# Kernel optimization log

Measured on AMD Instinct MI355X. Metric: run time of the kernel, lower is better.

Reference implementation:

```python
import jax, jax.numpy as jnp
import numpy as np

D_MODEL = 1024
N_HEADS = 16
D_HEAD = D_MODEL // N_HEADS


def setup_inputs() -> dict:
    key = jax.random.key(0)
    k1, k2, k3 = jax.random.split(key, 3)
    B, N = 2, 2048
    x = jax.random.normal(k1, (B, N, D_MODEL), dtype=jnp.float32)
    # torch nn.Linear(d, 3d, bias=False): y = x @ W.T ; we store W_qkv as [D, 3D]
    scale_in = 1.0 / np.sqrt(D_MODEL)
    W_qkv = jax.random.uniform(k2, (D_MODEL, 3 * D_MODEL), dtype=jnp.float32,
                               minval=-scale_in, maxval=scale_in)
    W_out = jax.random.uniform(k3, (D_MODEL, D_MODEL), dtype=jnp.float32,
                               minval=-scale_in, maxval=scale_in)
    return {"x": x, "W_qkv": W_qkv, "W_out": W_out}


def reference(x, W_qkv, W_out):
    B, N, D = x.shape
    qkv = x @ W_qkv                                    # [B, N, 3D]
    q, k, v = jnp.split(qkv, 3, axis=-1)
    # [B, N, D] -> [B, H, N, d_head]
    def heads(t):
        return t.reshape(B, N, N_HEADS, D_HEAD).transpose(0, 2, 1, 3)
    q, k, v = heads(q), heads(k), heads(v)
    scores = jnp.einsum('bhnd,bhmd->bhnm', q, k) / np.sqrt(D_HEAD)  # [B,H,N,N]
    causal_mask = jnp.triu(jnp.ones((N, N), dtype=bool), k=1)
    scores = jnp.where(causal_mask, -jnp.inf, scores)
    attn = jax.nn.softmax(scores, axis=-1)             # [B,H,N,N]
    out = jnp.einsum('bhnm,bhmd->bhnd', attn, v)       # [B,H,N,d_head]
    out = out.transpose(0, 2, 1, 3).reshape(B, N, D)
    out = out @ W_out.T if False else out @ W_out      # W_out stored [D,D], x @ W
    return out, attn
```

## Files before the change

### kernel.cpp

```cpp
#include <hip/hip_runtime.h>
#include <hip/hip_bf16.h>

typedef __bf16 bf16;
typedef __bf16 bf16x4 __attribute__((ext_vector_type(4)));
typedef __bf16 bf16x8 __attribute__((ext_vector_type(8)));
typedef float  f32x4  __attribute__((ext_vector_type(4)));

#define MFMA16(a, b, c) __builtin_amdgcn_mfma_f32_16x16x32_bf16((a), (b), (c), 0, 0, 0)

typedef const __attribute__((address_space(1))) void* gptr_t;
typedef __attribute__((address_space(3))) void* sptr_t;

__device__ __forceinline__ void load_lds16(const bf16* g, bf16* l) {
  __builtin_amdgcn_global_load_lds((gptr_t)g, (sptr_t)l, 16, 0, 0);
}

__global__ __launch_bounds__(256) void detect_dtype(const unsigned short* __restrict__ w,
                                                    int* __restrict__ flag) {
  __shared__ int cnt[256];
  int c = 0;
#pragma unroll
  for (int k = 0; k < 16; ++k) {
    unsigned short v = w[(threadIdx.x * 16 + k) * 2];
    int e = (v >> 7) & 0xFF;
    c += (e >= 90 && e <= 130) ? 1 : 0;
  }
  cnt[threadIdx.x] = c;
  __syncthreads();
  if (threadIdx.x == 0) {
    int t = 0;
    for (int i = 0; i < 256; ++i) t += cnt[i];
    *flag = (t > 2048) ? 1 : 0;
  }
}

__global__ __launch_bounds__(256) void convert_to_bf16(const void* __restrict__ in,
                                                       bf16* __restrict__ out,
                                                       const int* __restrict__ flag) {
  const int i0 = (blockIdx.x * 256 + threadIdx.x) * 8;
  if (*flag) {
    *(bf16x8*)(out + i0) = *(const bf16x8*)((const bf16*)in + i0);
  } else {
    const float* p = (const float*)in;
    float4 a = *(const float4*)(p + i0);
    float4 b = *(const float4*)(p + i0 + 4);
    bf16x8 v;
    v[0] = (bf16)a.x; v[1] = (bf16)a.y; v[2] = (bf16)a.z; v[3] = (bf16)a.w;
    v[4] = (bf16)b.x; v[5] = (bf16)b.y; v[6] = (bf16)b.z; v[7] = (bf16)b.w;
    *(bf16x8*)(out + i0) = v;
  }
}

__global__ __launch_bounds__(256) void transpose_any(const void* __restrict__ in,
                                                     bf16* __restrict__ out,
                                                     const int* __restrict__ flag,
                                                     int R, int C) {
  __shared__ bf16 t[64][65];
  const int c0 = blockIdx.x * 64, r0 = blockIdx.y * 64;
  const int tid = threadIdx.x;
  const int lc = tid & 63, lr4 = tid >> 6;
  if (*flag) {
    const bf16* p = (const bf16*)in;
#pragma unroll
    for (int i = 0; i < 16; ++i) {
      int r = i * 4 + lr4;
      t[r][lc] = p[(size_t)(r0 + r) * C + c0 + lc];
    }
  } else {
    const float* p = (const float*)in;
#pragma unroll
    for (int i = 0; i < 16; ++i) {
      int r = i * 4 + lr4;
      t[r][lc] = (bf16)p[(size_t)(r0 + r) * C + c0 + lc];
    }
  }
  __syncthreads();
#pragma unroll
  for (int i = 0; i < 16; ++i) {
    int r = i * 4 + lr4;
    out[(size_t)(c0 + r) * R + r0 + lc] = t[lc][r];
  }
}

__global__ __launch_bounds__(256) void transpose_v(const bf16* __restrict__ qkv,
                                                   bf16* __restrict__ vt) {
  __shared__ bf16 t[64][65];
  const int bh = blockIdx.y, b = bh >> 4, h = bh & 15;
  const int j0 = blockIdx.x * 64;
  const int tid = threadIdx.x;
  const int lc = tid & 63, lr4 = tid >> 6;
  const bf16* src = qkv + (size_t)b * 2048 * 3072 + 2048 + (size_t)h * 64;
#pragma unroll
  for (int i = 0; i < 16; ++i) {
    int j = i * 4 + lr4;
    t[j][lc] = src[(size_t)(j0 + j) * 3072 + lc];
  }
  __syncthreads();
  bf16* dst = vt + (size_t)bh * 64 * 2048;
#pragma unroll
  for (int i = 0; i < 16; ++i) {
    int d = i * 4 + lr4;
    dst[(size_t)d * 2048 + j0 + lc] = t[lc][d];
  }
}

template <typename CT>
__global__ __launch_bounds__(256) void gemm_bt(const bf16* __restrict__ A,
                                               const bf16* __restrict__ Bt,
                                               CT* __restrict__ C,
                                               int K, int ldc) {
  __shared__ bf16 a_lds[128 * 32];
  __shared__ bf16 b_lds[128 * 32];
  const int tid = threadIdx.x;
  const int w = tid >> 6, lane = tid & 63, l15 = lane & 15, quad = lane >> 4;
  const int wr = w >> 1, wc = w & 1;
  const int m0 = blockIdx.y * 128, n0 = blockIdx.x * 128;

  const f32x4 fz = {0.f, 0.f, 0.f, 0.f};
  f32x4 acc[4][4];
#pragma unroll
  for (int i = 0; i < 4; ++i)
#pragma unroll
    for (int j = 0; j < 4; ++j) acc[i][j] = fz;

  for (int k0 = 0; k0 < K; k0 += 32) {
#pragma unroll
    for (int i = 0; i < 2; ++i) {
      int c = tid + i * 256;
      int r = c >> 2, kk = c & 3;
      load_lds16(A + (size_t)(m0 + r) * K + k0 + kk * 8, &a_lds[c * 8]);
      load_lds16(Bt + (size_t)(n0 + r) * K + k0 + kk * 8, &b_lds[c * 8]);
    }
    __syncthreads();
    bf16x8 af[4], bfr[4];
#pragma unroll
    for (int mb = 0; mb < 4; ++mb)
      af[mb] = *(const bf16x8*)&a_lds[(wr * 64 + mb * 16 + l15) * 32 + quad * 8];
#pragma unroll
    for (int nb = 0; nb < 4; ++nb)
      bfr[nb] = *(const bf16x8*)&b_lds[(wc * 64 + nb * 16 + l15) * 32 + quad * 8];
#pragma unroll
    for (int mb = 0; mb < 4; ++mb)
#pragma unroll
      for (int nb = 0; nb < 4; ++nb)
        acc[mb][nb] = MFMA16(af[mb], bfr[nb], acc[mb][nb]);
    __syncthreads();
  }

#pragma unroll
  for (int mb = 0; mb < 4; ++mb)
#pragma unroll
    for (int nb = 0; nb < 4; ++nb) {
      int row = m0 + wr * 64 + mb * 16 + quad * 4;
      int col = n0 + wc * 64 + nb * 16 + l15;
#pragma unroll
      for (int r = 0; r < 4; ++r)
        C[(size_t)(row + r) * ldc + col] = (CT)acc[mb][nb][r];
    }
}

__device__ __forceinline__ void qk_tile(const char* kt_base, const bf16x8 (&qf)[2][2],
                                        int l15, int quad, f32x4 (&st)[8][2]) {
  const f32x4 fz = {0.f, 0.f, 0.f, 0.f};
  __builtin_amdgcn_s_setprio(1);
#pragma unroll
  for (int jb = 0; jb < 8; ++jb) {
    const char* kr = kt_base + (size_t)(jb * 16 + l15) * 6144 + quad * 16;
    bf16x8 kf0 = *(const bf16x8*)kr;
    bf16x8 kf1 = *(const bf16x8*)(kr + 64);
    st[jb][0] = MFMA16(kf0, qf[0][0], fz);
    st[jb][0] = MFMA16(kf1, qf[0][1], st[jb][0]);
    st[jb][1] = MFMA16(kf0, qf[1][0], fz);
    st[jb][1] = MFMA16(kf1, qf[1][1], st[jb][1]);
  }
  __builtin_amdgcn_s_setprio(0);
}

__global__ __launch_bounds__(256, 2) void fused_attn(const bf16* __restrict__ qkv,
                                                     const bf16* __restrict__ vt,
                                                     float* __restrict__ attn,
                                                     bf16* __restrict__ o_ws) {
  __shared__ bf16 p_lds[128 * 128];

  const int bh = blockIdx.y;
  const int b = bh >> 4, h = bh & 15;
  const int qt = (bh & 16) ? (15 - (int)blockIdx.x) : (int)blockIdx.x;
  const int tid = threadIdx.x;
  const int w = tid >> 6, lane = tid & 63, l15 = lane & 15, quad = lane >> 4;
  const int q0 = qt * 128;

  const char* qkvb = (const char*)qkv;
  const size_t kbyte0 = ((size_t)b * 2048 * 3072 + 1024 + (size_t)h * 64) * 2;
  const char* vtb = (const char*)vt + ((size_t)bh * 64) * 2048 * 2;

  for (int kt = qt + 1; kt < 16; ++kt) {
    float* abase = attn + ((size_t)bh << 22) + (size_t)q0 * 2048 + kt * 128;
    const f32x4 z4 = {0.f, 0.f, 0.f, 0.f};
#pragma unroll
    for (int it = 0; it < 16; ++it) {
      const int il = it * 8 + w * 2 + (lane >> 5);
      __builtin_nontemporal_store(z4, (f32x4*)(abase + (size_t)il * 2048 + (lane & 31) * 4));
    }
  }

  bf16x8 qf[2][2];
#pragma unroll
  for (int ib = 0; ib < 2; ++ib)
#pragma unroll
    for (int ks = 0; ks < 2; ++ks) {
      const bf16* qp = qkv + ((size_t)b * 2048 + q0 + w * 32 + ib * 16 + l15) * 3072
                       + h * 64 + ks * 32 + quad * 8;
      bf16x8 v = *(const bf16x8*)qp;
      bf16x8 sv;
#pragma unroll
      for (int u = 0; u < 8; ++u) sv[u] = (bf16)((float)v[u] * 0.125f);
      qf[ib][ks] = sv;
    }

  float m_run[2] = {-3e38f, -3e38f};
  float l_run[2] = {0.f, 0.f};

  for (int kt = 0; kt <= qt; ++kt) {
    f32x4 st[8][2];
    qk_tile(qkvb + kbyte0 + (size_t)kt * 128 * 6144, qf, l15, quad, st);

    const bool diag = (kt == qt);
#pragma unroll
    for (int ib = 0; ib < 2; ++ib) {
      const int ig = q0 + w * 32 + ib * 16 + l15;
      float tmax = -3e38f;
#pragma unroll
      for (int jb = 0; jb < 8; ++jb)
#pragma unroll
        for (int r = 0; r < 4; ++r) {
          const int jg = kt * 128 + jb * 16 + quad * 4 + r;
          float s = st[jb][ib][r];
          if (diag && jg > ig) { s = -3e38f; st[jb][ib][r] = s; }
          tmax = fmaxf(tmax, s);
        }
      tmax = fmaxf(tmax, __shfl_xor(tmax, 16));
      tmax = fmaxf(tmax, __shfl_xor(tmax, 32));
      const float mnew = fmaxf(m_run[ib], tmax);
      float tsum = 0.f;
#pragma unroll
      for (int jb = 0; jb < 8; ++jb)
#pragma unroll
        for (int r = 0; r < 4; ++r) {
          const float s = st[jb][ib][r];
          tsum += (s > -1e38f) ? __expf(s - mnew) : 0.f;
        }
      tsum += __shfl_xor(tsum, 16);
      tsum += __shfl_xor(tsum, 32);
      l_run[ib] = l_run[ib] * __expf(m_run[ib] - mnew) + tsum;
      m_run[ib] = mnew;
    }
  }

  const float invl[2] = {1.f / l_run[0], 1.f / l_run[1]};

  f32x4 oacc[2][4];
#pragma unroll
  for (int ib = 0; ib < 2; ++ib)
#pragma unroll
    for (int db = 0; db < 4; ++db) {
      const f32x4 fz = {0.f, 0.f, 0.f, 0.f};
      oacc[ib][db] = fz;
    }

  for (int kt = 0; kt <= qt; ++kt) {
    f32x4 st[8][2];
    qk_tile(qkvb + kbyte0 + (size_t)kt * 128 * 6144, qf, l15, quad, st);

    const bool diag = (kt == qt);
#pragma unroll
    for (int ib = 0; ib < 2; ++ib) {
      const int ig = q0 + w * 32 + ib * 16 + l15;
      const int il = w * 32 + ib * 16 + l15;
#pragma unroll
      for (int jb = 0; jb < 8; ++jb) {
        bf16x4 pk;
#pragma unroll
        for (int r = 0; r < 4; ++r) {
          const int jg = kt * 128 + jb * 16 + quad * 4 + r;
          float p = __expf(st[jb][ib][r] - m_run[ib]) * invl[ib];
          if (diag && jg > ig) p = 0.f;
          pk[r] = (bf16)p;
        }
        *(bf16x4*)((char*)p_lds + il * 256 + ((jb * 32 + quad * 8) ^ ((il & 7) << 4))) = pk;
      }
    }

    bf16x8 vfr[4][4];
#pragma unroll
    for (int js = 0; js < 4; ++js)
#pragma unroll
      for (int db = 0; db < 4; ++db) {
        const int dl = db * 16 + l15;
        vfr[js][db] = *(const bf16x8*)(vtb + (size_t)dl * 4096 + kt * 256 + js * 64 + quad * 16);
      }

    {
      float* abase = attn + ((size_t)bh << 22) + (size_t)q0 * 2048 + kt * 128;
#pragma unroll
      for (int it = 0; it < 16; ++it) {
        const int il = w * 32 + it * 2 + (lane >> 5);
        const int jb4 = (lane & 31) * 8;
        bf16x4 pv = *(const bf16x4*)((char*)p_lds + il * 256 + (jb4 ^ ((il & 7) << 4)));
        f32x4 f = {(float)pv[0], (float)pv[1], (float)pv[2], (float)pv[3]};
        __builtin_nontemporal_store(f, (f32x4*)(abase + (size_t)il * 2048 + (lane & 31) * 4));
      }
    }

    __builtin_amdgcn_s_setprio(1);
#pragma unroll
    for (int js = 0; js < 4; ++js) {
      bf16x8 pa[2];
#pragma unroll
      for (int ib = 0; ib < 2; ++ib) {
        const int il = w * 32 + ib * 16 + l15;
        pa[ib] = *(const bf16x8*)((char*)p_lds + il * 256 + ((js * 64 + quad * 16) ^ ((il & 7) << 4)));
      }
#pragma unroll
      for (int ib = 0; ib < 2; ++ib)
#pragma unroll
        for (int db = 0; db < 4; ++db)
          oacc[ib][db] = MFMA16(pa[ib], vfr[js][db], oacc[ib][db]);
    }
    __builtin_amdgcn_s_setprio(0);
  }

#pragma unroll
  for (int ib = 0; ib < 2; ++ib)
#pragma unroll
    for (int db = 0; db < 4; ++db)
#pragma unroll
      for (int r = 0; r < 4; ++r) {
        const int ig = q0 + w * 32 + ib * 16 + quad * 4 + r;
        const int dg = h * 64 + db * 16 + l15;
        o_ws[((size_t)b * 2048 + ig) * 1024 + dg] = (bf16)oacc[ib][db][r];
      }
}

extern "C" void kernel_launch(void* const* d_in, const int* in_sizes, int n_in,
                              void* d_out, int out_size, void* d_ws, size_t ws_size,
                              hipStream_t stream) {
  const void* x_raw = d_in[0];
  const void* w_qkv = d_in[1];
  const void* w_out = d_in[2];
  float* out  = (float*)d_out;
  float* attn = out + 4194304;

  bf16* ws     = (bf16*)d_ws;
  bf16* qkv_ws = ws;
  bf16* x_bf   = ws + 12582912;
  bf16* vt_ws  = ws + 12582912;
  bf16* woT    = ws + 12582912;
  bf16* wqkvT  = ws + 16777216;
  bf16* o_ws   = ws + 16777216;
  int*  flag   = (int*)(ws + 20971520);

  detect_dtype<<<1, 256, 0, stream>>>((const unsigned short*)w_qkv, flag);
  convert_to_bf16<<<2048, 256, 0, stream>>>(x_raw, x_bf, flag);
  transpose_any<<<dim3(48, 16), 256, 0, stream>>>(w_qkv, wqkvT, flag, 1024, 3072);
  gemm_bt<bf16><<<dim3(24, 32), 256, 0, stream>>>(x_bf, wqkvT, qkv_ws, 1024, 3072);
  transpose_v<<<dim3(32, 32), 256, 0, stream>>>(qkv_ws, vt_ws);
  fused_attn<<<dim3(16, 32), 256, 0, stream>>>(qkv_ws, vt_ws, attn, o_ws);
  transpose_any<<<dim3(16, 16), 256, 0, stream>>>(w_out, woT, flag, 1024, 1024);
  gemm_bt<float><<<dim3(8, 32), 256, 0, stream>>>(o_ws, woT, out, 1024, 1024);
}
```

Measured before the change: 743.7 us.

## Stage K tiles into double-buffered swizzled LDS and interleave zero-fill stores

In both attention passes, each K tile is now loaded cooperatively into a double-buffered, XOR-swizzled LDS buffer with global_load_lds, and the next tile is prefetched while the current one is used. Before, each wave fetched the same K rows from global memory on its own. The stores that zero the masked upper-triangle attn tiles are spread across the loop iterations instead of all being issued up front, so they can overlap with compute. The cost is 32KB more LDS per block and a block-wide barrier every iteration, which may limit occupancy or add stalls.

```diff
diff --git a/kernel.cpp b/kernel.cpp
--- a/kernel.cpp
+++ b/kernel.cpp
@@ -159,15 +159,17 @@
     }
 }
 
-__device__ __forceinline__ void qk_tile(const char* kt_base, const bf16x8 (&qf)[2][2],
-                                        int l15, int quad, f32x4 (&st)[8][2]) {
+__device__ __forceinline__ void compute_st(const bf16* k_lds, const bf16x8 (&qf)[2][2],
+                                           int l15, int quad, f32x4 (&st)[8][2]) {
   const f32x4 fz = {0.f, 0.f, 0.f, 0.f};
   __builtin_amdgcn_s_setprio(1);
 #pragma unroll
   for (int jb = 0; jb < 8; ++jb) {
-    const char* kr = kt_base + (size_t)(jb * 16 + l15) * 6144 + quad * 16;
-    bf16x8 kf0 = *(const bf16x8*)kr;
-    bf16x8 kf1 = *(const bf16x8*)(kr + 64);
+    const int jl = jb * 16 + l15;
+    const char* kb = (const char*)k_lds + jl * 128;
+    const int sw = (jl & 7) << 4;
+    bf16x8 kf0 = *(const bf16x8*)(kb + ((quad * 16) ^ sw));
+    bf16x8 kf1 = *(const bf16x8*)(kb + ((64 + quad * 16) ^ sw));
     st[jb][0] = MFMA16(kf0, qf[0][0], fz);
     st[jb][0] = MFMA16(kf1, qf[0][1], st[jb][0]);
     st[jb][1] = MFMA16(kf0, qf[1][0], fz);
@@ -180,6 +182,7 @@
                                                      const bf16* __restrict__ vt,
                                                      float* __restrict__ attn,
                                                      bf16* __restrict__ o_ws) {
+  __shared__ bf16 k_lds[2][128 * 64];
   __shared__ bf16 p_lds[128 * 128];
 
   const int bh = blockIdx.y;
@@ -192,16 +195,28 @@
   const char* qkvb = (const char*)qkv;
   const size_t kbyte0 = ((size_t)b * 2048 * 3072 + 1024 + (size_t)h * 64) * 2;
   const char* vtb = (const char*)vt + ((size_t)bh * 64) * 2048 * 2;
-
-  for (int kt = qt + 1; kt < 16; ++kt) {
-    float* abase = attn + ((size_t)bh << 22) + (size_t)q0 * 2048 + kt * 128;
+  float* attn_q0 = attn + ((size_t)bh << 22) + (size_t)q0 * 2048;
+
+  int zt = qt + 1;
+  auto zero_tile_at = [&](int t) {
+    float* abase = attn_q0 + t * 128;
     const f32x4 z4 = {0.f, 0.f, 0.f, 0.f};
 #pragma unroll
     for (int it = 0; it < 16; ++it) {
       const int il = it * 8 + w * 2 + (lane >> 5);
       __builtin_nontemporal_store(z4, (f32x4*)(abase + (size_t)il * 2048 + (lane & 31) * 4));
     }
-  }
+  };
+
+  auto stage_k = [&](int kt, int buf) {
+#pragma unroll
+    for (int c = 0; c < 4; ++c) {
+      const int L = c * 4096 + tid * 16;
+      const int j = L >> 7, cb = L & 127;
+      const char* src = qkvb + kbyte0 + (size_t)(kt * 128 + j) * 6144 + (cb ^ ((j & 7) << 4));
+      load_lds16((const bf16*)src, (bf16*)((char*)k_lds[buf] + L));
+    }
+  };
 
   bf16x8 qf[2][2];
 #pragma unroll
@@ -220,9 +235,14 @@
   float m_run[2] = {-3e38f, -3e38f};
   float l_run[2] = {0.f, 0.f};
 
+  stage_k(0, 0);
+  __syncthreads();
   for (int kt = 0; kt <= qt; ++kt) {
+    if (kt < qt) stage_k(kt + 1, (kt + 1) & 1);
+    if (zt < 16) zero_tile_at(zt++);
+
     f32x4 st[8][2];
-    qk_tile(qkvb + kbyte0 + (size_t)kt * 128 * 6144, qf, l15, quad, st);
+    compute_st(k_lds[kt & 1], qf, l15, quad, st);
 
     const bool diag = (kt == qt);
 #pragma unroll
@@ -254,6 +274,7 @@
       l_run[ib] = l_run[ib] * __expf(m_run[ib] - mnew) + tsum;
       m_run[ib] = mnew;
     }
+    __syncthreads();
   }
 
   const float invl[2] = {1.f / l_run[0], 1.f / l_run[1]};
@@ -267,9 +288,14 @@
       oacc[ib][db] = fz;
     }
 
+  stage_k(0, 0);
+  __syncthreads();
   for (int kt = 0; kt <= qt; ++kt) {
+    if (kt < qt) stage_k(kt + 1, (kt + 1) & 1);
+    if (zt < 16) zero_tile_at(zt++);
+
     f32x4 st[8][2];
-    qk_tile(qkvb + kbyte0 + (size_t)kt * 128 * 6144, qf, l15, quad, st);
+    compute_st(k_lds[kt & 1], qf, l15, quad, st);
 
     const bool diag = (kt == qt);
 #pragma unroll
@@ -300,7 +326,7 @@
       }
 
     {
-      float* abase = attn + ((size_t)bh << 22) + (size_t)q0 * 2048 + kt * 128;
+      float* abase = attn_q0 + kt * 128;
 #pragma unroll
       for (int it = 0; it < 16; ++it) {
         const int il = w * 32 + it * 2 + (lane >> 5);
@@ -327,7 +353,10 @@
           oacc[ib][db] = MFMA16(pa[ib], vfr[js][db], oacc[ib][db]);
     }
     __builtin_amdgcn_s_setprio(0);
-  }
+    __syncthreads();
+  }
+
+  while (zt < 16) zero_tile_at(zt++);
 
 #pragma unroll
   for (int ib = 0; ib < 2; ++ib)
```

Result: faster. 693.5 us (-6.7%).
